# Kernel tuning notes

Hardware: AMD Instinct MI355X
Metric: run time of the kernel (lower is better)

The kernel has to match this reference:

```python
import jax, jax.numpy as jnp
import numpy as np

EMBED = 1024
B, I, J = 8, 2048, 2048
SCALE = EMBED ** -0.5


def setup_inputs() -> dict:
    key = jax.random.key(0)
    ks = jax.random.split(key, 5)
    s = EMBED ** -0.5  # init scale for weights
    return {
        "q_in": jax.random.normal(ks[0], (B, I, EMBED), dtype=jnp.float32),
        "k_v": jax.random.normal(ks[1], (B, J, EMBED), dtype=jnp.float32),
        "Wq": jax.random.normal(ks[2], (EMBED, EMBED), dtype=jnp.float32) * s,
        "bq": jnp.zeros((EMBED,), dtype=jnp.float32),
        "Wk": jax.random.normal(ks[3], (EMBED, EMBED), dtype=jnp.float32) * s,
        "bk": jnp.zeros((EMBED,), dtype=jnp.float32),
        "Wv": jax.random.normal(ks[4], (EMBED, EMBED), dtype=jnp.float32) * s,
        "bv": jnp.zeros((EMBED,), dtype=jnp.float32),
    }


def reference(q_in, k_v, Wq, bq, Wk, bk, Wv, bv):
    # Linear projections (torch Linear: x @ W.T + b; here W stored as [in, out])
    q = q_in @ Wq + bq            # [b, i, d]
    k = k_v @ Wk + bk             # [b, j, d]
    v = k_v @ Wv + bv             # [b, j, d]
    sim = jnp.einsum('bid,bjd->bij', q, k) * SCALE  # [b, i, j]
    attn = jax.nn.softmax(sim, axis=-1)
    # dropout with drop_rate=0.0 is identity
    out = jnp.einsum('bij,bjd->bid', attn, v)       # [b, i, d]
    return out
```

## Files before the change

### kernel.cpp

```cpp
#include <hip/hip_runtime.h>
#include <hip/hip_bf16.h>


#define BATCH 8
#define SEQ   2048
#define EMB   1024
#define SC2   0.045084222f

typedef __attribute__((ext_vector_type(8))) short bf16x8;
typedef __attribute__((ext_vector_type(4))) float f32x4;
typedef __attribute__((ext_vector_type(4))) unsigned short u16x4;
typedef __attribute__((ext_vector_type(8))) unsigned short u16x8;
typedef __attribute__((ext_vector_type(4))) float fl4;

__device__ __forceinline__ unsigned short f2bf(float f) {
    unsigned u = __builtin_bit_cast(unsigned, f);
    unsigned r = u + 0x7fffu + ((u >> 16) & 1u);
    return (unsigned short)(r >> 16);
}
__device__ __forceinline__ float bf2f(unsigned short s) {
    return __builtin_bit_cast(float, ((unsigned)s) << 16);
}
__device__ __forceinline__ void gload16(const unsigned short* g, unsigned short* l) {
    __builtin_amdgcn_global_load_lds(
        (const __attribute__((address_space(1))) void*)g,
        (__attribute__((address_space(3))) void*)l, 16, 0, 0);
}

__global__ __launch_bounds__(256)
void convert_in(const float* __restrict__ q_in, const float* __restrict__ k_v,
                unsigned short* __restrict__ qbin, unsigned short* __restrict__ kvbin)
{
    const size_t N = (size_t)BATCH * SEQ * EMB;
    size_t idx = ((size_t)blockIdx.x * 256 + threadIdx.x) * 8;
    const size_t stride = (size_t)gridDim.x * 256 * 8;
    for (; idx < N; idx += stride) {
        fl4 a0 = *(const fl4*)&q_in[idx];
        fl4 a1 = *(const fl4*)&q_in[idx + 4];
        fl4 b0 = *(const fl4*)&k_v[idx];
        fl4 b1 = *(const fl4*)&k_v[idx + 4];
        u16x8 ua, ub;
#pragma unroll
        for (int i = 0; i < 4; i++) {
            ua[i] = f2bf(a0[i]); ua[i + 4] = f2bf(a1[i]);
            ub[i] = f2bf(b0[i]); ub[i + 4] = f2bf(b1[i]);
        }
        *(u16x8*)&qbin[idx] = ua;
        *(u16x8*)&kvbin[idx] = ub;
    }
}

__global__ __launch_bounds__(256)
void convert_w(const float* __restrict__ Wq, const float* __restrict__ Wk,
               const float* __restrict__ Wv, unsigned short* __restrict__ Wt)
{
    const int wsel = blockIdx.y;
    const float* W = (wsel == 0) ? Wq : (wsel == 1) ? Wk : Wv;
    unsigned short* O = Wt + (size_t)wsel * EMB * EMB;
    const int k0 = (blockIdx.x >> 4) * 64;
    const int n0 = (blockIdx.x & 15) * 64;
    __shared__ unsigned short l[64 * 65];
    const int tid = threadIdx.x;
#pragma unroll
    for (int it = 0; it < 16; it++) {
        const int lin = it * 256 + tid;
        const int k = lin >> 6, n = lin & 63;
        l[n * 65 + k] = f2bf(W[(size_t)(k0 + k) * EMB + n0 + n]);
    }
    __syncthreads();
#pragma unroll
    for (int it = 0; it < 16; it++) {
        const int lin = it * 256 + tid;
        const int n = lin >> 6, k = lin & 63;
        O[(size_t)(n0 + n) * EMB + k0 + k] = l[n * 65 + k];
    }
}

__global__ __launch_bounds__(256, 2)
void proj_q_kernel(const unsigned short* __restrict__ X,
                   const unsigned short* __restrict__ Wt,
                   const float* __restrict__ bias,
                   unsigned short* __restrict__ O)
{
    const int bid = blockIdx.x;
    const int mt = ((bid >> 6) << 3) | (bid & 7);
    const int nt = (bid >> 3) & 7;
    const int m0 = mt * 128, n0 = nt * 128;

    __shared__ unsigned short lA[128 * 64];
    __shared__ unsigned short lB[128 * 64];

    const int tid = threadIdx.x, lane = tid & 63;
    const int w = tid >> 6, wr = w >> 1, wc = w & 1;
    const int r = lane & 15, g = lane >> 4;
    const int srow = lane >> 3, scol = lane & 7;

    f32x4 acc[4][4];
#pragma unroll
    for (int i = 0; i < 4; i++)
#pragma unroll
        for (int j = 0; j < 4; j++) acc[i][j] = (f32x4)0.0f;

    for (int k0 = 0; k0 < EMB; k0 += 64) {
        __syncthreads();
#pragma unroll
        for (int i = 0; i < 4; i++) {
            const int c = w * 4 + i;
            const int row = c * 8 + srow;
            gload16(&X[(size_t)(m0 + row) * EMB + k0 + scol * 8], &lA[c * 512]);
            gload16(&Wt[(size_t)(n0 + row) * EMB + k0 + scol * 8], &lB[c * 512]);
        }
        __syncthreads();
#pragma unroll
        for (int kk = 0; kk < 2; kk++) {
            bf16x8 af[4], bf[4];
#pragma unroll
            for (int m = 0; m < 4; m++)
                af[m] = *(bf16x8*)&lA[(wr * 64 + m * 16 + r) * 64 + kk * 32 + g * 8];
#pragma unroll
            for (int n = 0; n < 4; n++)
                bf[n] = *(bf16x8*)&lB[(wc * 64 + n * 16 + r) * 64 + kk * 32 + g * 8];
#pragma unroll
            for (int m = 0; m < 4; m++)
#pragma unroll
                for (int n = 0; n < 4; n++)
                    acc[m][n] = __builtin_amdgcn_mfma_f32_16x16x32_bf16(af[m], bf[n], acc[m][n], 0, 0, 0);
        }
    }

#pragma unroll
    for (int n = 0; n < 4; n++) {
        const int col = n0 + wc * 64 + n * 16 + r;
        const float bb = bias[col];
#pragma unroll
        for (int m = 0; m < 4; m++) {
            const int rowb = m0 + wr * 64 + m * 16 + g * 4;
#pragma unroll
            for (int i = 0; i < 4; i++)
                O[(size_t)(rowb + i) * EMB + col] = f2bf(acc[m][n][i] + bb);
        }
    }
}

__global__ __launch_bounds__(256, 2)
void proj_kv_kernel(const unsigned short* __restrict__ X,
                    const unsigned short* __restrict__ Wkt,
                    const unsigned short* __restrict__ Wvt,
                    const float* __restrict__ bk, const float* __restrict__ bv,
                    unsigned short* __restrict__ kb, unsigned short* __restrict__ vt)
{
    const int bid = blockIdx.x;
    const int mt = ((bid >> 6) << 3) | (bid & 7);
    const int nt = (bid >> 3) & 7;
    const int m0 = mt * 128, n0 = nt * 128;

    __shared__ unsigned short lA[128 * 64];
    __shared__ unsigned short lBk[128 * 64];
    __shared__ unsigned short lBv[128 * 64];

    const int tid = threadIdx.x, lane = tid & 63;
    const int w = tid >> 6, wr = w >> 1, wc = w & 1;
    const int r = lane & 15, g = lane >> 4;
    const int srow = lane >> 3, scol = lane & 7;

    f32x4 acck[4][4], accv[4][4];
#pragma unroll
    for (int i = 0; i < 4; i++)
#pragma unroll
        for (int j = 0; j < 4; j++) { acck[i][j] = (f32x4)0.0f; accv[i][j] = (f32x4)0.0f; }

    for (int k0 = 0; k0 < EMB; k0 += 64) {
        __syncthreads();
#pragma unroll
        for (int i = 0; i < 4; i++) {
            const int c = w * 4 + i;
            const int row = c * 8 + srow;
            const size_t goff = (size_t)row * EMB + k0 + scol * 8;
            gload16(&X[(size_t)m0 * EMB + goff], &lA[c * 512]);
            gload16(&Wkt[(size_t)n0 * EMB + goff], &lBk[c * 512]);
            gload16(&Wvt[(size_t)n0 * EMB + goff], &lBv[c * 512]);
        }
        __syncthreads();
#pragma unroll
        for (int kk = 0; kk < 2; kk++) {
            bf16x8 af[4], bfk[4], bfv[4];
#pragma unroll
            for (int m = 0; m < 4; m++)
                af[m] = *(bf16x8*)&lA[(wr * 64 + m * 16 + r) * 64 + kk * 32 + g * 8];
#pragma unroll
            for (int n = 0; n < 4; n++) {
                bfk[n] = *(bf16x8*)&lBk[(wc * 64 + n * 16 + r) * 64 + kk * 32 + g * 8];
                bfv[n] = *(bf16x8*)&lBv[(wc * 64 + n * 16 + r) * 64 + kk * 32 + g * 8];
            }
#pragma unroll
            for (int m = 0; m < 4; m++)
#pragma unroll
                for (int n = 0; n < 4; n++) {
                    acck[m][n] = __builtin_amdgcn_mfma_f32_16x16x32_bf16(af[m], bfk[n], acck[m][n], 0, 0, 0);
                    accv[m][n] = __builtin_amdgcn_mfma_f32_16x16x32_bf16(af[m], bfv[n], accv[m][n], 0, 0, 0);
                }
        }
    }

    const int b = m0 >> 11;
    const int j0 = m0 & 2047;
#pragma unroll
    for (int n = 0; n < 4; n++) {
        const int col = n0 + wc * 64 + n * 16 + r;
        const float bbk = bk[col];
        const float bbv = bv[col];
#pragma unroll
        for (int m = 0; m < 4; m++) {
            const int rowb = m0 + wr * 64 + m * 16 + g * 4;
#pragma unroll
            for (int i = 0; i < 4; i++)
                kb[(size_t)(rowb + i) * EMB + col] = f2bf(acck[m][n][i] + bbk);
            const int j = j0 + wr * 64 + m * 16 + g * 4;
            u16x4 u;
#pragma unroll
            for (int i = 0; i < 4; i++) u[i] = f2bf(accv[m][n][i] + bbv);
            *(u16x4*)&vt[((size_t)b * EMB + col) * SEQ + j] = u;
        }
    }
}

#define QLDK 72

__global__ __launch_bounds__(256, 2)
void qk_kernel(const unsigned short* __restrict__ qb,
               const unsigned short* __restrict__ kb,
               unsigned short* __restrict__ P)
{
    const int b = blockIdx.z;
    const int m0 = blockIdx.x * 128;
    const int n0 = blockIdx.y * 128;
    const unsigned short* Aq = qb + (size_t)b * SEQ * EMB;
    const unsigned short* Bk = kb + (size_t)b * SEQ * EMB;

    __shared__ unsigned short lA[128 * QLDK];
    __shared__ unsigned short lB[128 * QLDK];

    const int tid = threadIdx.x, lane = tid & 63;
    const int w = tid >> 6, wr = w >> 1, wc = w & 1;
    const int r = lane & 15, g = lane >> 4;
    const int srow = tid >> 3, skc = tid & 7;

    f32x4 acc[4][4];
#pragma unroll
    for (int i = 0; i < 4; i++)
#pragma unroll
        for (int j = 0; j < 4; j++) acc[i][j] = (f32x4)0.0f;

    for (int k0 = 0; k0 < EMB; k0 += 64) {
        __syncthreads();
#pragma unroll
        for (int it = 0; it < 4; it++) {
            const int row = srow + it * 32;
            *(u16x8*)&lA[row * QLDK + skc * 8] =
                *(const u16x8*)&Aq[(size_t)(m0 + row) * EMB + k0 + skc * 8];
            *(u16x8*)&lB[row * QLDK + skc * 8] =
                *(const u16x8*)&Bk[(size_t)(n0 + row) * EMB + k0 + skc * 8];
        }
        __syncthreads();
#pragma unroll
        for (int kk = 0; kk < 2; kk++) {
            bf16x8 af[4], bfv[4];
#pragma unroll
            for (int m = 0; m < 4; m++)
                af[m] = *(bf16x8*)&lA[(wr * 64 + m * 16 + r) * QLDK + kk * 32 + g * 8];
#pragma unroll
            for (int n = 0; n < 4; n++)
                bfv[n] = *(bf16x8*)&lB[(wc * 64 + n * 16 + r) * QLDK + kk * 32 + g * 8];
#pragma unroll
            for (int m = 0; m < 4; m++)
#pragma unroll
                for (int n = 0; n < 4; n++)
                    acc[m][n] = __builtin_amdgcn_mfma_f32_16x16x32_bf16(af[m], bfv[n], acc[m][n], 0, 0, 0);
        }
    }

    unsigned short* Pb = P + (size_t)b * SEQ * SEQ;
#pragma unroll
    for (int m = 0; m < 4; m++) {
        const int ib = m0 + wr * 64 + m * 16 + g * 4;
#pragma unroll
        for (int n = 0; n < 4; n++) {
            const int j = n0 + wc * 64 + n * 16 + r;
#pragma unroll
            for (int i = 0; i < 4; i++) {
                const float p = exp2f(acc[m][n][i] * SC2);
                Pb[(size_t)(ib + i) * SEQ + j] = f2bf(p);
            }
        }
    }
}

__global__ __launch_bounds__(256)
void rowsum_kernel(const unsigned short* __restrict__ P, float* __restrict__ rs)
{
    const int row = blockIdx.x * 4 + (threadIdx.x >> 6);
    const int lane = threadIdx.x & 63;
    const unsigned short* p = P + (size_t)row * SEQ;
    float s = 0.f;
#pragma unroll
    for (int it = 0; it < 4; it++) {
        u16x8 u = *(const u16x8*)&p[it * 512 + lane * 8];
#pragma unroll
        for (int q = 0; q < 8; q++) s += bf2f(u[q]);
    }
#pragma unroll
    for (int off = 32; off > 0; off >>= 1) s += __shfl_down(s, off);
    if (lane == 0) rs[row] = s;
}

__global__ __launch_bounds__(256, 2)
void pv_kernel(const unsigned short* __restrict__ P,
               const unsigned short* __restrict__ vt,
               const float* __restrict__ rs,
               float* __restrict__ out)
{
    const int b = blockIdx.z;
    const int m0 = blockIdx.x * 128;
    const int n0 = blockIdx.y * 128;
    const unsigned short* Ap = P  + (size_t)b * SEQ * SEQ;
    const unsigned short* Bv = vt + (size_t)b * EMB * SEQ;

    __shared__ unsigned short lA[128 * QLDK];
    __shared__ unsigned short lB[128 * QLDK];

    const int tid = threadIdx.x, lane = tid & 63;
    const int w = tid >> 6, wr = w >> 1, wc = w & 1;
    const int r = lane & 15, g = lane >> 4;
    const int srow = tid >> 3, skc = tid & 7;

    f32x4 acc[4][4];
#pragma unroll
    for (int i = 0; i < 4; i++)
#pragma unroll
        for (int j = 0; j < 4; j++) acc[i][j] = (f32x4)0.0f;

    for (int k0 = 0; k0 < SEQ; k0 += 64) {
        __syncthreads();
#pragma unroll
        for (int it = 0; it < 4; it++) {
            const int row = srow + it * 32;
            *(u16x8*)&lA[row * QLDK + skc * 8] =
                *(const u16x8*)&Ap[(size_t)(m0 + row) * SEQ + k0 + skc * 8];
            *(u16x8*)&lB[row * QLDK + skc * 8] =
                *(const u16x8*)&Bv[(size_t)(n0 + row) * SEQ + k0 + skc * 8];
        }
        __syncthreads();
#pragma unroll
        for (int kk = 0; kk < 2; kk++) {
            bf16x8 af[4], bfv[4];
#pragma unroll
            for (int m = 0; m < 4; m++)
                af[m] = *(bf16x8*)&lA[(wr * 64 + m * 16 + r) * QLDK + kk * 32 + g * 8];
#pragma unroll
            for (int n = 0; n < 4; n++)
                bfv[n] = *(bf16x8*)&lB[(wc * 64 + n * 16 + r) * QLDK + kk * 32 + g * 8];
#pragma unroll
            for (int m = 0; m < 4; m++)
#pragma unroll
                for (int n = 0; n < 4; n++)
                    acc[m][n] = __builtin_amdgcn_mfma_f32_16x16x32_bf16(af[m], bfv[n], acc[m][n], 0, 0, 0);
        }
    }

    float* ob = out + (size_t)b * SEQ * EMB;
    const float* rsb = rs + (size_t)b * SEQ;
#pragma unroll
    for (int m = 0; m < 4; m++) {
        const int ib = m0 + wr * 64 + m * 16 + g * 4;
#pragma unroll
        for (int i = 0; i < 4; i++) {
            const float inv = 1.0f / rsb[ib + i];
#pragma unroll
            for (int n = 0; n < 4; n++) {
                const int d = n0 + wc * 64 + n * 16 + r;
                ob[(size_t)(ib + i) * EMB + d] = acc[m][n][i] * inv;
            }
        }
    }
}

extern "C" void kernel_launch(void* const* d_in, const int* in_sizes, int n_in,
                              void* d_out, int out_size, void* d_ws, size_t ws_size,
                              hipStream_t stream)
{
    const float* q_in = (const float*)d_in[0];
    const float* k_v  = (const float*)d_in[1];
    const float* Wq   = (const float*)d_in[2];
    const float* bq   = (const float*)d_in[3];
    const float* Wk   = (const float*)d_in[4];
    const float* bk   = (const float*)d_in[5];
    const float* Wv   = (const float*)d_in[6];
    const float* bv   = (const float*)d_in[7];
    float* out = (float*)d_out;

    char* ws = (char*)d_ws;
    unsigned short* qbin = (unsigned short*)(ws);
    unsigned short* kvbin= (unsigned short*)(ws + (size_t)33554432);
    unsigned short* P    = (unsigned short*)(ws);
    unsigned short* qb   = (unsigned short*)(ws + (size_t)67108864);
    unsigned short* kb   = (unsigned short*)(ws + (size_t)100663296);
    unsigned short* vt   = (unsigned short*)(ws + (size_t)134217728);
    unsigned short* Wt   = (unsigned short*)(ws + (size_t)167772160);
    float*          rs   = (float*)(ws + (size_t)174063616);

    convert_in<<<4096, 256, 0, stream>>>(q_in, k_v, qbin, kvbin);
    convert_w<<<dim3(256, 3), 256, 0, stream>>>(Wq, Wk, Wv, Wt);
    proj_q_kernel<<<1024, 256, 0, stream>>>(qbin, Wt, bq, qb);
    proj_kv_kernel<<<1024, 256, 0, stream>>>(kvbin, Wt + (size_t)EMB * EMB,
                                             Wt + (size_t)2 * EMB * EMB, bk, bv, kb, vt);
    qk_kernel<<<dim3(16, 16, BATCH), 256, 0, stream>>>(qb, kb, P);
    rowsum_kernel<<<dim3(4096), 256, 0, stream>>>(P, rs);
    pv_kernel<<<dim3(16, 8, BATCH), 256, 0, stream>>>(P, vt, rs, out);
}
```

Measured before the change: 353.0 us.

## Fuse softmax row sums into QK epilogue and use direct global-to-LDS loads

Row sums of the exponentials are now accumulated in the QK kernel epilogue via lane shuffles and written as per-column-tile partials, with a small final kernel reducing 32 partials per row. This replaces the separate rowsum pass that reread the whole bf16 P matrix. Both GEMM kernels now stage tiles through global_load_lds instead of register round-trips, and LDS rows lose their padding, which may introduce bank conflicts on the MFMA operand reads. Sums are taken from fp32 exponentials rather than rounded bf16 values, which differs slightly from the numerator.

```diff
diff --git a/kernel.cpp b/kernel.cpp
--- a/kernel.cpp
+++ b/kernel.cpp
@@ -224,12 +224,11 @@
     }
 }
 
-#define QLDK 72
-
 __global__ __launch_bounds__(256, 2)
 void qk_kernel(const unsigned short* __restrict__ qb,
                const unsigned short* __restrict__ kb,
-               unsigned short* __restrict__ P)
+               unsigned short* __restrict__ P,
+               float* __restrict__ Ppart)
 {
     const int b = blockIdx.z;
     const int m0 = blockIdx.x * 128;
@@ -237,13 +236,13 @@
     const unsigned short* Aq = qb + (size_t)b * SEQ * EMB;
     const unsigned short* Bk = kb + (size_t)b * SEQ * EMB;
 
-    __shared__ unsigned short lA[128 * QLDK];
-    __shared__ unsigned short lB[128 * QLDK];
+    __shared__ unsigned short lA[128 * 64];
+    __shared__ unsigned short lB[128 * 64];
 
     const int tid = threadIdx.x, lane = tid & 63;
     const int w = tid >> 6, wr = w >> 1, wc = w & 1;
     const int r = lane & 15, g = lane >> 4;
-    const int srow = tid >> 3, skc = tid & 7;
+    const int srow = lane >> 3, scol = lane & 7;
 
     f32x4 acc[4][4];
 #pragma unroll
@@ -254,12 +253,11 @@
     for (int k0 = 0; k0 < EMB; k0 += 64) {
         __syncthreads();
 #pragma unroll
-        for (int it = 0; it < 4; it++) {
-            const int row = srow + it * 32;
-            *(u16x8*)&lA[row * QLDK + skc * 8] =
-                *(const u16x8*)&Aq[(size_t)(m0 + row) * EMB + k0 + skc * 8];
-            *(u16x8*)&lB[row * QLDK + skc * 8] =
-                *(const u16x8*)&Bk[(size_t)(n0 + row) * EMB + k0 + skc * 8];
+        for (int i = 0; i < 4; i++) {
+            const int c = w * 4 + i;
+            const int row = c * 8 + srow;
+            gload16(&Aq[(size_t)(m0 + row) * EMB + k0 + scol * 8], &lA[c * 512]);
+            gload16(&Bk[(size_t)(n0 + row) * EMB + k0 + scol * 8], &lB[c * 512]);
         }
         __syncthreads();
 #pragma unroll
@@ -267,10 +265,10 @@
             bf16x8 af[4], bfv[4];
 #pragma unroll
             for (int m = 0; m < 4; m++)
-                af[m] = *(bf16x8*)&lA[(wr * 64 + m * 16 + r) * QLDK + kk * 32 + g * 8];
+                af[m] = *(bf16x8*)&lA[(wr * 64 + m * 16 + r) * 64 + kk * 32 + g * 8];
 #pragma unroll
             for (int n = 0; n < 4; n++)
-                bfv[n] = *(bf16x8*)&lB[(wc * 64 + n * 16 + r) * QLDK + kk * 32 + g * 8];
+                bfv[n] = *(bf16x8*)&lB[(wc * 64 + n * 16 + r) * 64 + kk * 32 + g * 8];
 #pragma unroll
             for (int m = 0; m < 4; m++)
 #pragma unroll
@@ -280,6 +278,12 @@
     }
 
     unsigned short* Pb = P + (size_t)b * SEQ * SEQ;
+    float ps[4][4];
+#pragma unroll
+    for (int m = 0; m < 4; m++)
+#pragma unroll
+        for (int i = 0; i < 4; i++) ps[m][i] = 0.f;
+
 #pragma unroll
     for (int m = 0; m < 4; m++) {
         const int ib = m0 + wr * 64 + m * 16 + g * 4;
@@ -289,28 +293,39 @@
 #pragma unroll
             for (int i = 0; i < 4; i++) {
                 const float p = exp2f(acc[m][n][i] * SC2);
+                ps[m][i] += p;
                 Pb[(size_t)(ib + i) * SEQ + j] = f2bf(p);
             }
         }
     }
+#pragma unroll
+    for (int off = 1; off < 16; off <<= 1)
+#pragma unroll
+        for (int m = 0; m < 4; m++)
+#pragma unroll
+            for (int i = 0; i < 4; i++)
+                ps[m][i] += __shfl_xor(ps[m][i], off);
+    if (r == 0) {
+        const int slot = blockIdx.y * 2 + wc;
+        float* pp = Ppart + (size_t)slot * (BATCH * SEQ) + (size_t)b * SEQ;
+#pragma unroll
+        for (int m = 0; m < 4; m++) {
+            const int row = m0 + wr * 64 + m * 16 + g * 4;
+#pragma unroll
+            for (int i = 0; i < 4; i++) pp[row + i] = ps[m][i];
+        }
+    }
 }
 
 __global__ __launch_bounds__(256)
-void rowsum_kernel(const unsigned short* __restrict__ P, float* __restrict__ rs)
-{
-    const int row = blockIdx.x * 4 + (threadIdx.x >> 6);
-    const int lane = threadIdx.x & 63;
-    const unsigned short* p = P + (size_t)row * SEQ;
+void rowsum_final(const float* __restrict__ Ppart, float* __restrict__ rs)
+{
+    const int row = blockIdx.x * 256 + threadIdx.x;
     float s = 0.f;
 #pragma unroll
-    for (int it = 0; it < 4; it++) {
-        u16x8 u = *(const u16x8*)&p[it * 512 + lane * 8];
-#pragma unroll
-        for (int q = 0; q < 8; q++) s += bf2f(u[q]);
-    }
-#pragma unroll
-    for (int off = 32; off > 0; off >>= 1) s += __shfl_down(s, off);
-    if (lane == 0) rs[row] = s;
+    for (int slot = 0; slot < 32; slot++)
+        s += Ppart[(size_t)slot * (BATCH * SEQ) + row];
+    rs[row] = s;
 }
 
 __global__ __launch_bounds__(256, 2)
@@ -325,13 +340,13 @@
     const unsigned short* Ap = P  + (size_t)b * SEQ * SEQ;
     const unsigned short* Bv = vt + (size_t)b * EMB * SEQ;
 
-    __shared__ unsigned short lA[128 * QLDK];
-    __shared__ unsigned short lB[128 * QLDK];
+    __shared__ unsigned short lA[128 * 64];
+    __shared__ unsigned short lB[128 * 64];
 
     const int tid = threadIdx.x, lane = tid & 63;
     const int w = tid >> 6, wr = w >> 1, wc = w & 1;
     const int r = lane & 15, g = lane >> 4;
-    const int srow = tid >> 3, skc = tid & 7;
+    const int srow = lane >> 3, scol = lane & 7;
 
     f32x4 acc[4][4];
 #pragma unroll
@@ -342,12 +357,11 @@
     for (int k0 = 0; k0 < SEQ; k0 += 64) {
         __syncthreads();
 #pragma unroll
-        for (int it = 0; it < 4; it++) {
-            const int row = srow + it * 32;
-            *(u16x8*)&lA[row * QLDK + skc * 8] =
-                *(const u16x8*)&Ap[(size_t)(m0 + row) * SEQ + k0 + skc * 8];
-            *(u16x8*)&lB[row * QLDK + skc * 8] =
-                *(const u16x8*)&Bv[(size_t)(n0 + row) * SEQ + k0 + skc * 8];
+        for (int i = 0; i < 4; i++) {
+            const int c = w * 4 + i;
+            const int row = c * 8 + srow;
+            gload16(&Ap[(size_t)(m0 + row) * SEQ + k0 + scol * 8], &lA[c * 512]);
+            gload16(&Bv[(size_t)(n0 + row) * SEQ + k0 + scol * 8], &lB[c * 512]);
         }
         __syncthreads();
 #pragma unroll
@@ -355,10 +369,10 @@
             bf16x8 af[4], bfv[4];
 #pragma unroll
             for (int m = 0; m < 4; m++)
-                af[m] = *(bf16x8*)&lA[(wr * 64 + m * 16 + r) * QLDK + kk * 32 + g * 8];
+                af[m] = *(bf16x8*)&lA[(wr * 64 + m * 16 + r) * 64 + kk * 32 + g * 8];
 #pragma unroll
             for (int n = 0; n < 4; n++)
-                bfv[n] = *(bf16x8*)&lB[(wc * 64 + n * 16 + r) * QLDK + kk * 32 + g * 8];
+                bfv[n] = *(bf16x8*)&lB[(wc * 64 + n * 16 + r) * 64 + kk * 32 + g * 8];
 #pragma unroll
             for (int m = 0; m < 4; m++)
 #pragma unroll
@@ -406,14 +420,15 @@
     unsigned short* kb   = (unsigned short*)(ws + (size_t)100663296);
     unsigned short* vt   = (unsigned short*)(ws + (size_t)134217728);
     unsigned short* Wt   = (unsigned short*)(ws + (size_t)167772160);
-    float*          rs   = (float*)(ws + (size_t)174063616);
+    float*          Ppart= (float*)(ws + (size_t)174063616);
+    float*          rs   = (float*)(ws + (size_t)176160768);
 
     convert_in<<<4096, 256, 0, stream>>>(q_in, k_v, qbin, kvbin);
     convert_w<<<dim3(256, 3), 256, 0, stream>>>(Wq, Wk, Wv, Wt);
     proj_q_kernel<<<1024, 256, 0, stream>>>(qbin, Wt, bq, qb);
     proj_kv_kernel<<<1024, 256, 0, stream>>>(kvbin, Wt + (size_t)EMB * EMB,
                                              Wt + (size_t)2 * EMB * EMB, bk, bv, kb, vt);
-    qk_kernel<<<dim3(16, 16, BATCH), 256, 0, stream>>>(qb, kb, P);
-    rowsum_kernel<<<dim3(4096), 256, 0, stream>>>(P, rs);
+    qk_kernel<<<dim3(16, 16, BATCH), 256, 0, stream>>>(qb, kb, P, Ppart);
+    rowsum_final<<<64, 256, 0, stream>>>(Ppart, rs);
     pv_kernel<<<dim3(16, 8, BATCH), 256, 0, stream>>>(P, vt, rs, out);
 }
```

Result: slower. 367.5 us (+4.1%).
